# Optimization experiments

Hardware: AMD Instinct MI355X
Metric: run time of the kernel (lower is better)

The kernel has to match this reference:

```python
import jax, jax.numpy as jnp
import numpy as np

B, D, O, E = 8192, 1024, 1024, 8

def setup_inputs() -> dict:
    key = jax.random.key(0)
    ks = jax.random.split(key, 5)
    s = 1.0 / np.sqrt(D)
    return {
        "x": jax.random.normal(ks[0], (B, D), dtype=jnp.float32),
        "Wg": jax.random.uniform(ks[1], (D, E), jnp.float32, -s, s),
        "bg": jax.random.uniform(ks[2], (E,), jnp.float32, -s, s),
        "We": jax.random.uniform(ks[3], (E, D, O), jnp.float32, -s, s),
        "be": jax.random.uniform(ks[4], (E, O), jnp.float32, -s, s),
    }

def reference(x, Wg, bg, We, be):
    # gating: [B, E], softmax over experts (dim=1)
    gates = jax.nn.softmax(x @ Wg + bg, axis=1)
    # dense expert outputs: [B, E, O] (single batched GEMM over all experts)
    expert_out = jnp.einsum('bd,edo->beo', x, We) + be[None, :, :]
    # softmax-weighted combine (bmm of [B,1,E] @ [B,E,O] -> [B,O])
    return jnp.einsum('be,beo->bo', gates, expert_out)
```

## Files before the change

### kernel.cpp

```cpp
#include <hip/hip_runtime.h>
#include <hip/hip_bf16.h>
#include <stdint.h>

#define B_SZ 8192
#define D_SZ 1024
#define O_SZ 1024
#define E_SZ 8

typedef __bf16 bf16_t;
typedef __bf16 bf16x8 __attribute__((ext_vector_type(8)));
typedef __bf16 bf16x4 __attribute__((ext_vector_type(4)));
typedef float  f32x4  __attribute__((ext_vector_type(4)));

__global__ __launch_bounds__(256) void gating_kernel(
    const float* __restrict__ x, const float* __restrict__ Wg,
    const float* __restrict__ bg, float* __restrict__ gates) {
  const int w = threadIdx.x >> 6, lane = threadIdx.x & 63;
  const int b = blockIdx.x * 4 + w;
  const float* xr = x + (size_t)b * D_SZ;
  float acc[8];
#pragma unroll
  for (int e = 0; e < 8; ++e) acc[e] = 0.f;
  for (int it = 0; it < 16; ++it) {
    int d = it * 64 + lane;
    float xv = xr[d];
    const float4* wr = (const float4*)(Wg + d * 8);
    float4 w0 = wr[0], w1 = wr[1];
    acc[0] += xv * w0.x; acc[1] += xv * w0.y;
    acc[2] += xv * w0.z; acc[3] += xv * w0.w;
    acc[4] += xv * w1.x; acc[5] += xv * w1.y;
    acc[6] += xv * w1.z; acc[7] += xv * w1.w;
  }
#pragma unroll
  for (int off = 32; off >= 1; off >>= 1) {
#pragma unroll
    for (int e = 0; e < 8; ++e) acc[e] += __shfl_xor(acc[e], off, 64);
  }
  if (lane == 0) {
#pragma unroll
    for (int e = 0; e < 8; ++e) acc[e] += bg[e];
    float m = acc[0];
#pragma unroll
    for (int e = 1; e < 8; ++e) m = fmaxf(m, acc[e]);
    float s = 0.f, ex[8];
#pragma unroll
    for (int e = 0; e < 8; ++e) { ex[e] = __expf(acc[e] - m); s += ex[e]; }
    float inv = 1.0f / s;
    float* gr = gates + (size_t)b * 8;
#pragma unroll
    for (int e = 0; e < 8; ++e) gr[e] = ex[e] * inv;
  }
}

__global__ __launch_bounds__(256) void cvt_x_kernel(
    const float* __restrict__ x, bf16_t* __restrict__ xb) {
  size_t i = (size_t)blockIdx.x * 256 + threadIdx.x;
  float4 v = ((const float4*)x)[i];
  bf16x4 o;
  o[0] = (bf16_t)v.x; o[1] = (bf16_t)v.y; o[2] = (bf16_t)v.z; o[3] = (bf16_t)v.w;
  ((bf16x4*)xb)[i] = o;
}

__global__ __launch_bounds__(256) void transpose_we(
    const float* __restrict__ We, bf16_t* __restrict__ WeT) {
  __shared__ float tile[64][65];
  const int e = blockIdx.z;
  const int d0 = blockIdx.y * 64, o0 = blockIdx.x * 64;
  const int tx = threadIdx.x & 63, ty = threadIdx.x >> 6;
  const float* src = We + (size_t)e * D_SZ * O_SZ;
#pragma unroll
  for (int i = 0; i < 16; ++i) {
    int d = ty + i * 4;
    tile[d][tx] = src[(size_t)(d0 + d) * O_SZ + o0 + tx];
  }
  __syncthreads();
  bf16_t* dst = WeT + (size_t)e * O_SZ * D_SZ;
#pragma unroll
  for (int i = 0; i < 16; ++i) {
    int o = ty + i * 4;
    dst[(size_t)(o0 + o) * D_SZ + d0 + tx] = (bf16_t)tile[tx][o];
  }
}

__device__ __forceinline__ void gload_lds16(const bf16_t* g, char* l) {
  __builtin_amdgcn_global_load_lds(
      (const __attribute__((address_space(1))) void*)g,
      (__attribute__((address_space(3))) void*)l, 16, 0, 0);
}

__global__ __launch_bounds__(256, 2) void moe_gemm(
    const bf16_t* __restrict__ xb,
    const bf16_t* __restrict__ wet,
    const float* __restrict__ gates,
    const float* __restrict__ be,
    float* __restrict__ out)
{
  __shared__ bf16_t lA[128 * 32];
  __shared__ bf16_t lB[128 * 32];
  __shared__ float  lG[128 * 8];

  const int tid = threadIdx.x;
  const int b0 = blockIdx.y * 128;
  const int o0 = blockIdx.x * 128;

  {
    const float* gsrc = gates + (size_t)b0 * 8;
#pragma unroll
    for (int i = 0; i < 4; ++i) lG[tid + 256 * i] = gsrc[tid + 256 * i];
  }

  const int w = tid >> 6;
  const int lane = tid & 63;
  const int wm = (w >> 1) * 64;
  const int wn = (w & 1) * 64;
  const int m16 = lane & 15;
  const int q = lane >> 4;

  const int gi0 = tid, gi1 = tid + 256;
  const int ar0 = gi0 >> 2, ac0 = (((gi0 & 3) ^ ((gi0 >> 3) & 3)) * 8);
  const int ar1 = gi1 >> 2, ac1 = (((gi1 & 3) ^ ((gi1 >> 3) & 3)) * 8);
  char* lA0 = (char*)lA + w * 64 * 16;
  char* lA1 = (char*)lA + (256 + w * 64) * 16;
  char* lB0 = (char*)lB + w * 64 * 16;
  char* lB1 = (char*)lB + (256 + w * 64) * 16;

  const bf16_t* Abase = xb + (size_t)b0 * D_SZ;

  f32x4 outAcc[4][4];
#pragma unroll
  for (int i = 0; i < 4; ++i)
#pragma unroll
    for (int j = 0; j < 4; ++j) outAcc[i][j] = f32x4{0.f, 0.f, 0.f, 0.f};

  for (int e = 0; e < E_SZ; ++e) {
    const bf16_t* Bbase = wet + ((size_t)e * O_SZ + o0) * D_SZ;
    f32x4 acc[4][4];
#pragma unroll
    for (int i = 0; i < 4; ++i)
#pragma unroll
      for (int j = 0; j < 4; ++j) acc[i][j] = f32x4{0.f, 0.f, 0.f, 0.f};

    for (int kt = 0; kt < D_SZ / 32; ++kt) {
      const int kc = kt * 32;
      __syncthreads();
      gload_lds16(Abase + (size_t)ar0 * D_SZ + kc + ac0, lA0);
      gload_lds16(Abase + (size_t)ar1 * D_SZ + kc + ac1, lA1);
      gload_lds16(Bbase + (size_t)ar0 * D_SZ + kc + ac0, lB0);
      gload_lds16(Bbase + (size_t)ar1 * D_SZ + kc + ac1, lB1);
      __syncthreads();

      bf16x8 af[4], bf[4];
#pragma unroll
      for (int i = 0; i < 4; ++i) {
        int r = wm + i * 16 + m16;
        int pg = (q ^ ((r >> 1) & 3)) * 8;
        af[i] = *(const bf16x8*)&lA[r * 32 + pg];
      }
#pragma unroll
      for (int j = 0; j < 4; ++j) {
        int r = wn + j * 16 + m16;
        int pg = (q ^ ((r >> 1) & 3)) * 8;
        bf[j] = *(const bf16x8*)&lB[r * 32 + pg];
      }
#pragma unroll
      for (int i = 0; i < 4; ++i)
#pragma unroll
        for (int j = 0; j < 4; ++j)
          acc[i][j] = __builtin_amdgcn_mfma_f32_16x16x32_bf16(
              af[i], bf[j], acc[i][j], 0, 0, 0);
    }

#pragma unroll
    for (int j = 0; j < 4; ++j) {
      float bec = be[e * O_SZ + o0 + wn + j * 16 + m16];
#pragma unroll
      for (int i = 0; i < 4; ++i) {
#pragma unroll
        for (int rg = 0; rg < 4; ++rg) {
          float gv = lG[(wm + i * 16 + q * 4 + rg) * 8 + e];
          outAcc[i][j][rg] += gv * (acc[i][j][rg] + bec);
        }
      }
    }
  }

#pragma unroll
  for (int i = 0; i < 4; ++i)
#pragma unroll
    for (int rg = 0; rg < 4; ++rg) {
      float* orow = out + (size_t)(b0 + wm + i * 16 + q * 4 + rg) * O_SZ
                    + o0 + wn + m16;
#pragma unroll
      for (int j = 0; j < 4; ++j) orow[j * 16] = outAcc[i][j][rg];
    }
}

extern "C" void kernel_launch(void* const* d_in, const int* in_sizes, int n_in,
                              void* d_out, int out_size, void* d_ws, size_t ws_size,
                              hipStream_t stream) {
  const float* x  = (const float*)d_in[0];
  const float* Wg = (const float*)d_in[1];
  const float* bg = (const float*)d_in[2];
  const float* We = (const float*)d_in[3];
  const float* be = (const float*)d_in[4];
  float* out = (float*)d_out;

  char* ws = (char*)d_ws;
  float*  gates = (float*)ws;
  bf16_t* xb    = (bf16_t*)(ws + (1 << 18));
  bf16_t* wet   = (bf16_t*)(ws + (1 << 18) + (1 << 24));

  gating_kernel<<<B_SZ / 4, 256, 0, stream>>>(x, Wg, bg, gates);
  cvt_x_kernel<<<(B_SZ * D_SZ) / (4 * 256), 256, 0, stream>>>(x, xb);
  transpose_we<<<dim3(O_SZ / 64, D_SZ / 64, E_SZ), 256, 0, stream>>>(We, wet);
  moe_gemm<<<dim3(O_SZ / 128, B_SZ / 128), 256, 0, stream>>>(xb, wet, gates, be, out);
}
```

Baseline: 299.9 us.

## Fuse gating with bf16 conversion and pipeline MoE GEMM with triple-buffered LDS

The gating kernel now also writes the bf16 copy of x, so x is read once and one launch goes away. The GEMM moves to 256x128 tiles with 512 threads and BK=64. It runs a flattened loop over experts and K with a 3-stage global-to-LDS async pipeline: waits use vmcnt instead of full double syncs, and the gate and bias values sit in LDS. This is meant to hide memory latency and cut barrier overhead. The cost is more LDS per block, which may lower occupancy, plus hand-written waitcnt logic that can be fragile.

```diff
diff --git a/kernel.cpp b/kernel.cpp
--- a/kernel.cpp
+++ b/kernel.cpp
@@ -7,29 +7,45 @@
 #define O_SZ 1024
 #define E_SZ 8
 
+#define BM 256
+#define BN 128
+#define BK 64
+#define NT 128
+
 typedef __bf16 bf16_t;
 typedef __bf16 bf16x8 __attribute__((ext_vector_type(8)));
 typedef __bf16 bf16x4 __attribute__((ext_vector_type(4)));
 typedef float  f32x4  __attribute__((ext_vector_type(4)));
 
-__global__ __launch_bounds__(256) void gating_kernel(
+__global__ __launch_bounds__(256) void gating_cvt_kernel(
     const float* __restrict__ x, const float* __restrict__ Wg,
-    const float* __restrict__ bg, float* __restrict__ gates) {
+    const float* __restrict__ bg, float* __restrict__ gates,
+    bf16_t* __restrict__ xb) {
   const int w = threadIdx.x >> 6, lane = threadIdx.x & 63;
   const int b = blockIdx.x * 4 + w;
-  const float* xr = x + (size_t)b * D_SZ;
+  const float4* xr = (const float4*)(x + (size_t)b * D_SZ);
+  bf16x4* xbr = (bf16x4*)(xb + (size_t)b * D_SZ);
   float acc[8];
 #pragma unroll
   for (int e = 0; e < 8; ++e) acc[e] = 0.f;
-  for (int it = 0; it < 16; ++it) {
-    int d = it * 64 + lane;
-    float xv = xr[d];
-    const float4* wr = (const float4*)(Wg + d * 8);
-    float4 w0 = wr[0], w1 = wr[1];
-    acc[0] += xv * w0.x; acc[1] += xv * w0.y;
-    acc[2] += xv * w0.z; acc[3] += xv * w0.w;
-    acc[4] += xv * w1.x; acc[5] += xv * w1.y;
-    acc[6] += xv * w1.z; acc[7] += xv * w1.w;
+#pragma unroll 1
+  for (int it = 0; it < 4; ++it) {
+    int d4 = it * 64 + lane;
+    float4 v = xr[d4];
+    bf16x4 ob;
+    ob[0] = (bf16_t)v.x; ob[1] = (bf16_t)v.y;
+    ob[2] = (bf16_t)v.z; ob[3] = (bf16_t)v.w;
+    xbr[d4] = ob;
+    const float4* wr = (const float4*)(Wg + (size_t)d4 * 32);
+    float xs[4] = {v.x, v.y, v.z, v.w};
+#pragma unroll
+    for (int rr = 0; rr < 4; ++rr) {
+      float4 wa = wr[rr * 2], wb = wr[rr * 2 + 1];
+      acc[0] += xs[rr] * wa.x; acc[1] += xs[rr] * wa.y;
+      acc[2] += xs[rr] * wa.z; acc[3] += xs[rr] * wa.w;
+      acc[4] += xs[rr] * wb.x; acc[5] += xs[rr] * wb.y;
+      acc[6] += xs[rr] * wb.z; acc[7] += xs[rr] * wb.w;
+    }
   }
 #pragma unroll
   for (int off = 32; off >= 1; off >>= 1) {
@@ -50,15 +66,6 @@
 #pragma unroll
     for (int e = 0; e < 8; ++e) gr[e] = ex[e] * inv;
   }
-}
-
-__global__ __launch_bounds__(256) void cvt_x_kernel(
-    const float* __restrict__ x, bf16_t* __restrict__ xb) {
-  size_t i = (size_t)blockIdx.x * 256 + threadIdx.x;
-  float4 v = ((const float4*)x)[i];
-  bf16x4 o;
-  o[0] = (bf16_t)v.x; o[1] = (bf16_t)v.y; o[2] = (bf16_t)v.z; o[3] = (bf16_t)v.w;
-  ((bf16x4*)xb)[i] = o;
 }
 
 __global__ __launch_bounds__(256) void transpose_we(
@@ -82,107 +89,148 @@
   }
 }
 
-__device__ __forceinline__ void gload_lds16(const bf16_t* g, char* l) {
+__device__ __forceinline__ void gl16(const bf16_t* g, const bf16_t* l) {
   __builtin_amdgcn_global_load_lds(
       (const __attribute__((address_space(1))) void*)g,
       (__attribute__((address_space(3))) void*)l, 16, 0, 0);
 }
 
-__global__ __launch_bounds__(256, 2) void moe_gemm(
+__global__ __launch_bounds__(512, 2) void moe_gemm(
     const bf16_t* __restrict__ xb,
     const bf16_t* __restrict__ wet,
     const float* __restrict__ gates,
     const float* __restrict__ be,
     float* __restrict__ out)
 {
-  __shared__ bf16_t lA[128 * 32];
-  __shared__ bf16_t lB[128 * 32];
-  __shared__ float  lG[128 * 8];
+  __shared__ bf16_t lA[3][BM * BK];
+  __shared__ bf16_t lB[3][BN * BK];
+  __shared__ float  lG[BM * 9];
+  __shared__ float  lBe[E_SZ * BN];
 
   const int tid = threadIdx.x;
-  const int b0 = blockIdx.y * 128;
-  const int o0 = blockIdx.x * 128;
+  const int w = tid >> 6, lane = tid & 63;
+  const int b0 = blockIdx.y * BM;
+  const int o0 = blockIdx.x * BN;
+  const int wm = (w >> 1) * 64, wn = (w & 1) * 64;
+  const int m16 = lane & 15, q = lane >> 4;
 
   {
-    const float* gsrc = gates + (size_t)b0 * 8;
-#pragma unroll
-    for (int i = 0; i < 4; ++i) lG[tid + 256 * i] = gsrc[tid + 256 * i];
-  }
-
-  const int w = tid >> 6;
-  const int lane = tid & 63;
-  const int wm = (w >> 1) * 64;
-  const int wn = (w & 1) * 64;
-  const int m16 = lane & 15;
-  const int q = lane >> 4;
-
-  const int gi0 = tid, gi1 = tid + 256;
-  const int ar0 = gi0 >> 2, ac0 = (((gi0 & 3) ^ ((gi0 >> 3) & 3)) * 8);
-  const int ar1 = gi1 >> 2, ac1 = (((gi1 & 3) ^ ((gi1 >> 3) & 3)) * 8);
-  char* lA0 = (char*)lA + w * 64 * 16;
-  char* lA1 = (char*)lA + (256 + w * 64) * 16;
-  char* lB0 = (char*)lB + w * 64 * 16;
-  char* lB1 = (char*)lB + (256 + w * 64) * 16;
-
-  const bf16_t* Abase = xb + (size_t)b0 * D_SZ;
-
-  f32x4 outAcc[4][4];
+    float4 g4 = ((const float4*)(gates + (size_t)b0 * 8))[tid];
+    int gr = tid >> 1, gc = (tid & 1) * 4;
+    lG[gr * 9 + gc + 0] = g4.x; lG[gr * 9 + gc + 1] = g4.y;
+    lG[gr * 9 + gc + 2] = g4.z; lG[gr * 9 + gc + 3] = g4.w;
+#pragma unroll
+    for (int p = 0; p < 2; ++p) {
+      int idx = tid + p * 512;
+      lBe[idx] = be[(size_t)(idx >> 7) * O_SZ + o0 + (idx & 127)];
+    }
+  }
+
+  const bf16_t* aptr[4]; int aoffL[4];
+#pragma unroll
+  for (int j = 0; j < 4; ++j) {
+    int g0 = w * 64 + 512 * j;
+    int row = (g0 >> 3) + (lane >> 3);
+    int ls = (lane & 7) ^ (row & 7);
+    aptr[j] = xb + (size_t)(b0 + row) * D_SZ + ls * 8;
+    aoffL[j] = g0 * 8;
+  }
+  const bf16_t* bptr[2]; int boffL[2];
+#pragma unroll
+  for (int j = 0; j < 2; ++j) {
+    int g0 = w * 64 + 512 * j;
+    int row = (g0 >> 3) + (lane >> 3);
+    int ls = (lane & 7) ^ (row & 7);
+    bptr[j] = wet + (size_t)(o0 + row) * D_SZ + ls * 8;
+    boffL[j] = g0 * 8;
+  }
+
+#define STAGE(t_, buf_) do {                                                   \
+    const int kk_ = ((t_) & 15) << 6;                                          \
+    const size_t eo_ = (((size_t)((t_) >> 4)) << 20) + kk_;                    \
+    _Pragma("unroll")                                                          \
+    for (int js = 0; js < 4; ++js) gl16(aptr[js] + kk_, &lA[buf_][0] + aoffL[js]); \
+    _Pragma("unroll")                                                          \
+    for (int js = 0; js < 2; ++js) gl16(bptr[js] + eo_, &lB[buf_][0] + boffL[js]); \
+  } while (0)
+
+  f32x4 acc[4][4], outAcc[4][4];
 #pragma unroll
   for (int i = 0; i < 4; ++i)
 #pragma unroll
-    for (int j = 0; j < 4; ++j) outAcc[i][j] = f32x4{0.f, 0.f, 0.f, 0.f};
-
-  for (int e = 0; e < E_SZ; ++e) {
-    const bf16_t* Bbase = wet + ((size_t)e * O_SZ + o0) * D_SZ;
-    f32x4 acc[4][4];
-#pragma unroll
-    for (int i = 0; i < 4; ++i)
-#pragma unroll
-      for (int j = 0; j < 4; ++j) acc[i][j] = f32x4{0.f, 0.f, 0.f, 0.f};
-
-    for (int kt = 0; kt < D_SZ / 32; ++kt) {
-      const int kc = kt * 32;
-      __syncthreads();
-      gload_lds16(Abase + (size_t)ar0 * D_SZ + kc + ac0, lA0);
-      gload_lds16(Abase + (size_t)ar1 * D_SZ + kc + ac1, lA1);
-      gload_lds16(Bbase + (size_t)ar0 * D_SZ + kc + ac0, lB0);
-      gload_lds16(Bbase + (size_t)ar1 * D_SZ + kc + ac1, lB1);
-      __syncthreads();
-
-      bf16x8 af[4], bf[4];
-#pragma unroll
-      for (int i = 0; i < 4; ++i) {
-        int r = wm + i * 16 + m16;
-        int pg = (q ^ ((r >> 1) & 3)) * 8;
-        af[i] = *(const bf16x8*)&lA[r * 32 + pg];
-      }
-#pragma unroll
-      for (int j = 0; j < 4; ++j) {
-        int r = wn + j * 16 + m16;
-        int pg = (q ^ ((r >> 1) & 3)) * 8;
-        bf[j] = *(const bf16x8*)&lB[r * 32 + pg];
-      }
-#pragma unroll
-      for (int i = 0; i < 4; ++i)
-#pragma unroll
-        for (int j = 0; j < 4; ++j)
-          acc[i][j] = __builtin_amdgcn_mfma_f32_16x16x32_bf16(
-              af[i], bf[j], acc[i][j], 0, 0, 0);
-    }
-
-#pragma unroll
     for (int j = 0; j < 4; ++j) {
-      float bec = be[e * O_SZ + o0 + wn + j * 16 + m16];
-#pragma unroll
-      for (int i = 0; i < 4; ++i) {
-#pragma unroll
-        for (int rg = 0; rg < 4; ++rg) {
-          float gv = lG[(wm + i * 16 + q * 4 + rg) * 8 + e];
-          outAcc[i][j][rg] += gv * (acc[i][j][rg] + bec);
-        }
-      }
-    }
-  }
+      acc[i][j] = f32x4{0.f, 0.f, 0.f, 0.f};
+      outAcc[i][j] = f32x4{0.f, 0.f, 0.f, 0.f};
+    }
+
+  STAGE(0, 0);
+  STAGE(1, 1);
+  asm volatile("s_waitcnt lgkmcnt(0)" ::: "memory");
+
+#define BODY(cur_) do {                                                        \
+    const bf16_t* la_ = &lA[cur_][0];                                          \
+    const bf16_t* lb_ = &lB[cur_][0];                                          \
+    bf16x8 bfr[4][2];                                                          \
+    _Pragma("unroll")                                                          \
+    for (int j = 0; j < 4; ++j) {                                              \
+      int r = wn + j * 16 + m16;                                               \
+      const char* rb = (const char*)lb_ + r * 128;                             \
+      bfr[j][0] = *(const bf16x8*)(rb + (((q) ^ (r & 7)) << 4));               \
+      bfr[j][1] = *(const bf16x8*)(rb + (((4 | q) ^ (r & 7)) << 4));           \
+    }                                                                          \
+    _Pragma("unroll")                                                          \
+    for (int i = 0; i < 4; ++i) {                                              \
+      int r = wm + i * 16 + m16;                                               \
+      const char* ra = (const char*)la_ + r * 128;                             \
+      bf16x8 a0 = *(const bf16x8*)(ra + (((q) ^ (r & 7)) << 4));               \
+      bf16x8 a1 = *(const bf16x8*)(ra + (((4 | q) ^ (r & 7)) << 4));           \
+      _Pragma("unroll")                                                        \
+      for (int j = 0; j < 4; ++j) {                                            \
+        acc[i][j] = __builtin_amdgcn_mfma_f32_16x16x32_bf16(                   \
+            a0, bfr[j][0], acc[i][j], 0, 0, 0);                                \
+        acc[i][j] = __builtin_amdgcn_mfma_f32_16x16x32_bf16(                   \
+            a1, bfr[j][1], acc[i][j], 0, 0, 0);                                \
+      }                                                                        \
+    }                                                                          \
+  } while (0)
+
+#define COMBINE(e_) do {                                                       \
+    float bec_[4];                                                             \
+    _Pragma("unroll")                                                          \
+    for (int j = 0; j < 4; ++j) bec_[j] = lBe[(e_) * BN + wn + j * 16 + m16];  \
+    _Pragma("unroll")                                                          \
+    for (int i = 0; i < 4; ++i) {                                              \
+      _Pragma("unroll")                                                        \
+      for (int rg = 0; rg < 4; ++rg) {                                         \
+        float gv = lG[(wm + i * 16 + q * 4 + rg) * 9 + (e_)];                  \
+        _Pragma("unroll")                                                      \
+        for (int j = 0; j < 4; ++j) {                                          \
+          outAcc[i][j][rg] += gv * (acc[i][j][rg] + bec_[j]);                  \
+          acc[i][j][rg] = 0.f;                                                 \
+        }                                                                      \
+      }                                                                        \
+    }                                                                          \
+  } while (0)
+
+  int cur = 0;
+#pragma unroll 1
+  for (int t = 0; t < NT - 1; ++t) {
+    asm volatile("s_waitcnt vmcnt(6)" ::: "memory");
+    __builtin_amdgcn_s_barrier();
+    asm volatile("" ::: "memory");
+    if (t <= NT - 3) {
+      int nb = cur + 2; if (nb >= 3) nb -= 3;
+      STAGE(t + 2, nb);
+    }
+    BODY(cur);
+    if ((t & 15) == 15) COMBINE(t >> 4);
+    ++cur; if (cur == 3) cur = 0;
+  }
+  asm volatile("s_waitcnt vmcnt(0)" ::: "memory");
+  __builtin_amdgcn_s_barrier();
+  asm volatile("" ::: "memory");
+  BODY(cur);
+  COMBINE(7);
 
 #pragma unroll
   for (int i = 0; i < 4; ++i)
@@ -210,8 +258,7 @@
   bf16_t* xb    = (bf16_t*)(ws + (1 << 18));
   bf16_t* wet   = (bf16_t*)(ws + (1 << 18) + (1 << 24));
 
-  gating_kernel<<<B_SZ / 4, 256, 0, stream>>>(x, Wg, bg, gates);
-  cvt_x_kernel<<<(B_SZ * D_SZ) / (4 * 256), 256, 0, stream>>>(x, xb);
+  gating_cvt_kernel<<<B_SZ / 4, 256, 0, stream>>>(x, Wg, bg, gates, xb);
   transpose_we<<<dim3(O_SZ / 64, D_SZ / 64, E_SZ), 256, 0, stream>>>(We, wet);
-  moe_gemm<<<dim3(O_SZ / 128, B_SZ / 128), 256, 0, stream>>>(xb, wet, gates, be, out);
-}
+  moe_gemm<<<dim3(O_SZ / BN, B_SZ / BM), 512, 0, stream>>>(xb, wet, gates, be, out);
+}
```

Result: no change. 302.3 us (+0.8%).
